# Optimization experiments

Measured on AMD Instinct MI355X. Metric: run time of the kernel, lower is better.

## Reference

```python
import jax, jax.numpy as jnp
from jax import lax
import numpy as np

EPS = 1e-8
B, SA, SB = 32, 64, 64
H, WD, L, V, CLS = 128, 300, 20, 50000, 3


def _div(n, d):
    # faithful to div_with_small_value: clamp denominator at EPS
    return n / jnp.where(d > EPS, d, EPS)


def _lstm(x, Wih, Whh, bih, bhh):
    # PyTorch gate order: i, f, g, o. x: [B, S, D] -> outputs [B, S, H], last h [B, H]
    def step(carry, xt):
        h, c = carry
        g = xt @ Wih.T + bih + h @ Whh.T + bhh
        i, f, gg, o = jnp.split(g, 4, axis=-1)
        c = jax.nn.sigmoid(f) * c + jax.nn.sigmoid(i) * jnp.tanh(gg)
        h = jax.nn.sigmoid(o) * jnp.tanh(c)
        return (h, c), h
    h0 = jnp.zeros((x.shape[0], Whh.shape[1]), x.dtype)
    (hT, _), hs = lax.scan(step, (h0, h0), jnp.swapaxes(x, 0, 1))
    return jnp.swapaxes(hs, 0, 1), hT


def _bilstm(x, pf, pb):
    of, _ = _lstm(x, *pf)
    ob, _ = _lstm(x[:, ::-1], *pb)
    return jnp.concatenate([of, ob[:, ::-1]], axis=-1)


def _full_match(v1, v2, w):
    # v1: [B,S,H]; v2: [B,H] or [B,S,H]; w: [L,H] -> [B,S,L]
    v1p = v1[:, :, None, :] * w
    v2p = (v2[:, None, None, :] if v2.ndim == 2 else v2[:, :, None, :]) * w
    num = jnp.sum(v1p * v2p, -1)
    den = jnp.linalg.norm(v1p, axis=-1) * jnp.linalg.norm(v2p, axis=-1)
    return _div(num, den)


def _maxpool_match(v1, v2, w):
    # cosine between every (i, j) pair under each perspective -> [B,SA,SB,L]
    v1p = v1[:, :, None, :] * w  # [B,SA,L,H]
    v2p = v2[:, :, None, :] * w  # [B,SB,L,H]
    num = jnp.einsum('bild,bjld->bijl', v1p, v2p)
    den = jnp.linalg.norm(v1p, axis=-1)[:, :, None, :] * jnp.linalg.norm(v2p, axis=-1)[:, None, :, :]
    return _div(num, den)


def _attention(v1, v2):
    # cosine similarity matrix [B,SA,SB]
    num = jnp.einsum('bid,bjd->bij', v1, v2)
    den = jnp.linalg.norm(v1, axis=-1)[:, :, None] * jnp.linalg.norm(v2, axis=-1)[:, None, :]
    return _div(num, den)


def setup_inputs():
    key = jax.random.key(0)
    ks = iter(jax.random.split(key, 64))
    def nrm(shape, s=0.05):
        return jax.random.normal(next(ks), shape, jnp.float32) * s
    inp = {
        'Atoken': jax.random.randint(next(ks), (B, SA), 0, V),
        'Btoken': jax.random.randint(next(ks), (B, SB), 0, V),
        'word_emb': nrm((V, WD), 0.1),
    }
    for d in ('f', 'b'):
        inp['ctx_Wih_' + d] = nrm((4 * H, WD))
        inp['ctx_Whh_' + d] = nrm((4 * H, H))
        inp['ctx_bih_' + d] = jnp.zeros(4 * H, jnp.float32)
        inp['ctx_bhh_' + d] = jnp.zeros(4 * H, jnp.float32)
        inp['agg_Wih_' + d] = nrm((4 * H, 8 * L))
        inp['agg_Whh_' + d] = nrm((4 * H, H))
        inp['agg_bih_' + d] = jnp.zeros(4 * H, jnp.float32)
        inp['agg_bhh_' + d] = jnp.zeros(4 * H, jnp.float32)
    for i in range(1, 9):
        inp['mp_w%d' % i] = nrm((L, H), 0.1)
    inp['fc1_W'] = nrm((2 * H, 4 * H))
    inp['fc1_b'] = jnp.zeros(2 * H, jnp.float32)
    inp['fc2_W'] = nrm((CLS, 2 * H))
    inp['fc2_b'] = jnp.zeros(CLS, jnp.float32)
    return inp


def reference(Atoken, Btoken, word_emb,
              ctx_Wih_f, ctx_Whh_f, ctx_bih_f, ctx_bhh_f,
              ctx_Wih_b, ctx_Whh_b, ctx_bih_b, ctx_bhh_b,
              mp_w1, mp_w2, mp_w3, mp_w4, mp_w5, mp_w6, mp_w7, mp_w8,
              agg_Wih_f, agg_Whh_f, agg_bih_f, agg_bhh_f,
              agg_Wih_b, agg_Whh_b, agg_bih_b, agg_bhh_b,
              fc1_W, fc1_b, fc2_W, fc2_b):
    A = word_emb[Atoken]   # [B,SA,WD]
    Bx = word_emb[Btoken]  # [B,SB,WD]
    pf = (ctx_Wih_f, ctx_Whh_f, ctx_bih_f, ctx_bhh_f)
    pb = (ctx_Wih_b, ctx_Whh_b, ctx_bih_b, ctx_bhh_b)
    cA = _bilstm(A, pf, pb)
    cB = _bilstm(Bx, pf, pb)
    cA_f, cA_b = cA[..., :H], cA[..., H:]
    cB_f, cB_b = cB[..., :H], cB[..., H:]

    # full matching against last fw / first bw states
    mvA_full_f = _full_match(cA_f, cB_f[:, -1], mp_w1)
    mvA_full_b = _full_match(cA_b, cB_b[:, 0], mp_w2)
    mvB_full_f = _full_match(cB_f, cA_f[:, -1], mp_w1)
    mvB_full_b = _full_match(cB_b, cA_b[:, 0], mp_w2)

    # max-pooling matching
    mm_f = _maxpool_match(cA_f, cB_f, mp_w3)  # [B,SA,SB,L]
    mm_b = _maxpool_match(cA_b, cB_b, mp_w4)
    mvA_max_f = mm_f.max(2); mvA_max_b = mm_b.max(2)
    mvB_max_f = mm_f.max(1); mvB_max_b = mm_b.max(1)

    # attentive matching
    att_f = _attention(cA_f, cB_f)  # [B,SA,SB]
    att_b = _attention(cA_b, cB_b)
    mean_B_f = _div(jnp.einsum('bij,bjd->bid', att_f, cB_f), att_f.sum(2, keepdims=True))
    mean_B_b = _div(jnp.einsum('bij,bjd->bid', att_b, cB_b), att_b.sum(2, keepdims=True))
    mean_A_f = _div(jnp.einsum('bij,bid->bjd', att_f, cA_f), att_f.sum(1)[:, :, None])
    mean_A_b = _div(jnp.einsum('bij,bid->bjd', att_b, cA_b), att_b.sum(1)[:, :, None])
    mvA_am_f = _full_match(cA_f, mean_B_f, mp_w5)
    mvA_am_b = _full_match(cA_b, mean_B_b, mp_w6)
    mvB_am_f = _full_match(cB_f, mean_A_f, mp_w5)
    mvB_am_b = _full_match(cB_b, mean_A_b, mp_w6)

    # attentive-max matching (broadcast-multiply-reduce, the headroom hotspot)
    max_B_f = jnp.max(cB_f[:, None, :, :] * att_f[..., None], axis=2)  # [B,SA,H]
    max_B_b = jnp.max(cB_b[:, None, :, :] * att_b[..., None], axis=2)
    max_A_f = jnp.max(cA_f[:, :, None, :] * att_f[..., None], axis=1)  # [B,SB,H]
    max_A_b = jnp.max(cA_b[:, :, None, :] * att_b[..., None], axis=1)
    mvA_ax_f = _full_match(cA_f, max_B_f, mp_w7)
    mvA_ax_b = _full_match(cA_b, max_B_b, mp_w8)
    mvB_ax_f = _full_match(cB_f, max_A_f, mp_w7)
    mvB_ax_b = _full_match(cB_b, max_A_b, mp_w8)

    mvA = jnp.concatenate([mvA_full_f, mvA_max_f, mvA_am_f, mvA_ax_f,
                           mvA_full_b, mvA_max_b, mvA_am_b, mvA_ax_b], axis=2)  # [B,SA,8L]
    mvB = jnp.concatenate([mvB_full_f, mvB_max_f, mvB_am_f, mvB_ax_f,
                           mvB_full_b, mvB_max_b, mvB_am_b, mvB_ax_b], axis=2)

    apf = (agg_Wih_f, agg_Whh_f, agg_bih_f, agg_bhh_f)
    apb = (agg_Wih_b, agg_Whh_b, agg_bih_b, agg_bhh_b)
    _, hAf = _lstm(mvA, *apf); _, hAb = _lstm(mvA[:, ::-1], *apb)
    _, hBf = _lstm(mvB, *apf); _, hBb = _lstm(mvB[:, ::-1], *apb)
    out = jnp.concatenate([hAf, hAb, hBf, hBb], axis=1)  # [B, 4H]
    out = jnp.tanh(out @ fc1_W.T + fc1_b)
    logits = out @ fc2_W.T + fc2_b
    return jax.nn.softmax(logits, axis=-1)
```

## Files before the change

### kernel.cpp

```cpp
#include <hip/hip_runtime.h>
#include <math.h>


#define EPSV 1e-8f

__device__ __forceinline__ float sigm(float x) { return 1.f / (1.f + __expf(-x)); }
__device__ __forceinline__ float tanh_f(float x) {
    float t = expm1f(-2.f * fabsf(x));
    float r = -t / (t + 2.f);
    return copysignf(r, x);
}
__device__ __forceinline__ float divg(float n, float d) { return n / (d > EPSV ? d : EPSV); }

template<bool GATHER>
__global__ __launch_bounds__(256)
void gemm_gin(const float* __restrict__ X,
              const int* __restrict__ tokA, const int* __restrict__ tokB,
              const float* __restrict__ emb,
              const float* __restrict__ Wf, const float* __restrict__ Wb,
              const float* __restrict__ bihF, const float* __restrict__ bhhF,
              const float* __restrict__ bihB, const float* __restrict__ bhhB,
              int K, float* __restrict__ Gout)
{
    const int tid = threadIdx.x;
    const int tx = tid & 15, ty = tid >> 4;
    const int m0 = blockIdx.x * 64;
    const int n0 = blockIdx.y * 64;
    const int dir = (n0 >= 512) ? 1 : 0;
    const float* Wd = dir ? Wb : Wf;
    const int nn0 = n0 & 511;

    __shared__ __align__(16) float As[100 * 68];
    __shared__ __align__(16) float Bs[100 * 68];

    float acc[4][4];
#pragma unroll
    for (int r = 0; r < 4; ++r)
#pragma unroll
        for (int c = 0; c < 4; ++c) acc[r][c] = 0.f;

    for (int k0 = 0; k0 < K; k0 += 100) {
        int kc = K - k0; if (kc > 100) kc = 100;
        for (int e = tid; e < 64 * kc; e += 256) {
            int r = e / kc, c = e - r * kc;
            int m = m0 + r;
            const float* xrow;
            if (GATHER) {
                int tok = (m < 2048) ? tokA[m] : tokB[m - 2048];
                xrow = emb + (size_t)tok * 300;
            } else {
                xrow = X + (size_t)m * K;
            }
            As[c * 68 + r] = xrow[k0 + c];
        }
        for (int e = tid; e < 64 * kc; e += 256) {
            int r = e / kc, c = e - r * kc;
            Bs[c * 68 + r] = Wd[(size_t)(nn0 + r) * K + k0 + c];
        }
        __syncthreads();
#pragma unroll 4
        for (int k = 0; k < kc; ++k) {
            float4 a = *(const float4*)(As + k * 68 + (ty << 2));
            float4 b = *(const float4*)(Bs + k * 68 + (tx << 2));
            acc[0][0] += a.x * b.x; acc[0][1] += a.x * b.y; acc[0][2] += a.x * b.z; acc[0][3] += a.x * b.w;
            acc[1][0] += a.y * b.x; acc[1][1] += a.y * b.y; acc[1][2] += a.y * b.z; acc[1][3] += a.y * b.w;
            acc[2][0] += a.z * b.x; acc[2][1] += a.z * b.y; acc[2][2] += a.z * b.z; acc[2][3] += a.z * b.w;
            acc[3][0] += a.w * b.x; acc[3][1] += a.w * b.y; acc[3][2] += a.w * b.z; acc[3][3] += a.w * b.w;
        }
        __syncthreads();
    }

    const float* bih = dir ? bihB : bihF;
    const float* bhh = dir ? bhhB : bhhF;
    const int chain = ((m0 >= 2048) ? 2 : 0) + dir;
    const int nn = nn0 + (tx << 2);
    float b0 = bih[nn] + bhh[nn];
    float b1 = bih[nn + 1] + bhh[nn + 1];
    float b2 = bih[nn + 2] + bhh[nn + 2];
    float b3 = bih[nn + 3] + bhh[nn + 3];
#pragma unroll
    for (int r = 0; r < 4; ++r) {
        int m = m0 + (ty << 2) + r;
        int row = m & 2047;
        float4 o;
        o.x = acc[r][0] + b0; o.y = acc[r][1] + b1; o.z = acc[r][2] + b2; o.w = acc[r][3] + b3;
        *(float4*)(Gout + ((size_t)chain * 2048 + row) * 512 + nn) = o;
    }
}

__global__ __launch_bounds__(512, 2)
void lstm_kernel(const float* __restrict__ Gin,
                 const float* __restrict__ WhhF, const float* __restrict__ WhhB,
                 float* __restrict__ outH, float* __restrict__ hfin, int storeAll)
{
    const int tid = threadIdx.x;
    const int chain = blockIdx.x >> 5;
    const int b = blockIdx.x & 31;
    const int rev = chain & 1;
    const float* Whh = rev ? WhhB : WhhF;

    __shared__ float4 hs4[32];
    __shared__ float gact[512];
    float* hs = (float*)hs4;

    float4 w4[32];
    const float4* wrow = (const float4*)(Whh + (size_t)tid * 128);
#pragma unroll
    for (int q = 0; q < 32; ++q) w4[q] = wrow[q];

    if (tid < 32) hs4[tid] = make_float4(0.f, 0.f, 0.f, 0.f);
    float c_reg = 0.f;
    __syncthreads();

    const size_t base = ((size_t)chain * 32 + b) * 64;
    float gin_cur = Gin[(base + (rev ? 63 : 0)) * 512 + tid];

    for (int t = 0; t < 64; ++t) {
        const int s_cur = rev ? 63 - t : t;
        float gin_next = 0.f;
        if (t + 1 < 64) {
            int s_next = rev ? 62 - t : t + 1;
            gin_next = Gin[(base + s_next) * 512 + tid];
        }
        float a0 = 0.f, a1 = 0.f, a2 = 0.f, a3 = 0.f;
#pragma unroll
        for (int q = 0; q < 32; ++q) {
            float4 h4 = hs4[q];
            a0 += h4.x * w4[q].x; a1 += h4.y * w4[q].y;
            a2 += h4.z * w4[q].z; a3 += h4.w * w4[q].w;
        }
        float g = gin_cur + ((a0 + a1) + (a2 + a3));
        gact[tid] = ((tid >> 7) == 2) ? tanh_f(g) : sigm(g);
        __syncthreads();
        if (tid < 128) {
            float iv = gact[tid], fv = gact[128 + tid], gv = gact[256 + tid], ov = gact[384 + tid];
            c_reg = fv * c_reg + iv * gv;
            float hv = ov * tanh_f(c_reg);
            hs[tid] = hv;
            if (storeAll) outH[(base + s_cur) * 128 + tid] = hv;
        }
        __syncthreads();
        gin_cur = gin_next;
    }
    if (!storeAll && tid < 128) hfin[(size_t)b * 512 + chain * 128 + tid] = hs[tid];
}

__global__ __launch_bounds__(256)
void attn_kernel(const float* __restrict__ ctxH, float* __restrict__ att)
{
    const int tid = threadIdx.x;
    const int b = blockIdx.x;
    const int dir = blockIdx.y;
    const float* cA = ctxH + (((size_t)dir * 32 + b) * 64) * 128;
    const float* cB = ctxH + (((size_t)(2 + dir) * 32 + b) * 64) * 128;
    __shared__ __align__(16) float sa[64 * 132];
    __shared__ __align__(16) float sb[64 * 132];
    __shared__ float na[64], nb[64];

    for (int e = tid; e < 8192; e += 256) {
        int i = e >> 7, k = e & 127;
        sa[i * 132 + k] = cA[e];
        sb[i * 132 + k] = cB[e];
    }
    __syncthreads();
    if (tid < 64) {
        float s = 0.f;
        for (int k = 0; k < 128; ++k) { float v = sa[tid * 132 + k]; s += v * v; }
        na[tid] = sqrtf(s);
    } else if (tid < 128) {
        int j = tid - 64; float s = 0.f;
        for (int k = 0; k < 128; ++k) { float v = sb[j * 132 + k]; s += v * v; }
        nb[j] = sqrtf(s);
    }
    __syncthreads();

    const int tx = tid & 15, ty = tid >> 4;
    float acc[4][4] = {};
    for (int k4 = 0; k4 < 32; ++k4) {
        float4 av[4], bv[4];
#pragma unroll
        for (int r = 0; r < 4; ++r) av[r] = *(const float4*)(sa + ((ty << 2) + r) * 132 + (k4 << 2));
#pragma unroll
        for (int c = 0; c < 4; ++c) bv[c] = *(const float4*)(sb + ((tx << 2) + c) * 132 + (k4 << 2));
#pragma unroll
        for (int r = 0; r < 4; ++r)
#pragma unroll
            for (int c = 0; c < 4; ++c)
                acc[r][c] += av[r].x * bv[c].x + av[r].y * bv[c].y + av[r].z * bv[c].z + av[r].w * bv[c].w;
    }
    float* attb = att + (((size_t)dir * 32 + b) * 64) * 64;
#pragma unroll
    for (int r = 0; r < 4; ++r) {
        int i = (ty << 2) + r;
#pragma unroll
        for (int c = 0; c < 4; ++c) {
            int j = (tx << 2) + c;
            attb[i * 64 + j] = divg(acc[r][c], na[i] * nb[j]);
        }
    }
}

__global__ __launch_bounds__(256)
void meanmax_kernel(const float* __restrict__ ctxH, const float* __restrict__ att,
                    float* __restrict__ meanB, float* __restrict__ meanA,
                    float* __restrict__ maxB, float* __restrict__ maxA)
{
    const int tid = threadIdx.x;
    const int b = blockIdx.x, dir = blockIdx.y, side = blockIdx.z;
    __shared__ float sat[64 * 68];
    __shared__ __align__(16) float sc[64 * 132];
    __shared__ float ssum[64];

    const float* attb = att + (((size_t)dir * 32 + b) * 64) * 64;
    const int chain_src = side ? dir : (2 + dir);
    const float* cS = ctxH + (((size_t)chain_src * 32 + b) * 64) * 128;

    for (int e = tid; e < 4096; e += 256) sat[(e >> 6) * 68 + (e & 63)] = attb[e];
    for (int e = tid; e < 8192; e += 256) sc[(e >> 7) * 132 + (e & 127)] = cS[e];
    __syncthreads();
    if (tid < 64) {
        float s = 0.f;
        for (int q = 0; q < 64; ++q) s += side ? sat[q * 68 + tid] : sat[tid * 68 + q];
        ssum[tid] = s;
    }
    __syncthreads();

    const int r = tid >> 2;
    const int d0 = (tid & 3) * 32;
    float4 am[8], axv[8];
#pragma unroll
    for (int p = 0; p < 8; ++p) {
        am[p] = make_float4(0.f, 0.f, 0.f, 0.f);
        axv[p] = make_float4(-INFINITY, -INFINITY, -INFINITY, -INFINITY);
    }
    for (int q = 0; q < 64; ++q) {
        float a = side ? sat[q * 68 + r] : sat[r * 68 + q];
#pragma unroll
        for (int p = 0; p < 8; ++p) {
            float4 cv = *(const float4*)(sc + q * 132 + d0 + (p << 2));
            float px = a * cv.x, py = a * cv.y, pz = a * cv.z, pw = a * cv.w;
            am[p].x += px; am[p].y += py; am[p].z += pz; am[p].w += pw;
            axv[p].x = fmaxf(axv[p].x, px); axv[p].y = fmaxf(axv[p].y, py);
            axv[p].z = fmaxf(axv[p].z, pz); axv[p].w = fmaxf(axv[p].w, pw);
        }
    }
    float den = ssum[r] > EPSV ? ssum[r] : EPSV;
    float inv = 1.f / den;
    float* mout = (side ? meanA : meanB) + (((size_t)dir * 32 + b) * 64 + r) * 128 + d0;
    float* xout = (side ? maxA : maxB) + (((size_t)dir * 32 + b) * 64 + r) * 128 + d0;
#pragma unroll
    for (int p = 0; p < 8; ++p) {
        float4 o;
        o.x = am[p].x * inv; o.y = am[p].y * inv; o.z = am[p].z * inv; o.w = am[p].w * inv;
        *(float4*)(mout + (p << 2)) = o;
        *(float4*)(xout + (p << 2)) = axv[p];
    }
}

__global__ __launch_bounds__(256)
void mm_kernel(const float* __restrict__ ctxH,
               const float* __restrict__ mpw3, const float* __restrict__ mpw4,
               float* __restrict__ mvA, float* __restrict__ mvB)
{
    const int tid = threadIdx.x;
    const int b = blockIdx.x, l = blockIdx.y, dir = blockIdx.z;
    const float* wsrc = (dir ? mpw4 : mpw3) + (size_t)l * 128;
    __shared__ float wl[128];
    __shared__ __align__(16) float su[64 * 132];
    __shared__ __align__(16) float sv[64 * 132];
    __shared__ float nu[64], nv[64];
    __shared__ float smm[64 * 68];

    const float* cA = ctxH + (((size_t)dir * 32 + b) * 64) * 128;
    const float* cB = ctxH + (((size_t)(2 + dir) * 32 + b) * 64) * 128;

    if (tid < 128) wl[tid] = wsrc[tid];
    __syncthreads();
    for (int e = tid; e < 8192; e += 256) {
        int i = e >> 7, k = e & 127;
        float w = wl[k];
        su[i * 132 + k] = cA[e] * w;
        sv[i * 132 + k] = cB[e] * w;
    }
    __syncthreads();
    if (tid < 64) {
        float s = 0.f;
        for (int k = 0; k < 128; ++k) { float v = su[tid * 132 + k]; s += v * v; }
        nu[tid] = sqrtf(s);
    } else if (tid < 128) {
        int j = tid - 64; float s = 0.f;
        for (int k = 0; k < 128; ++k) { float v = sv[j * 132 + k]; s += v * v; }
        nv[j] = sqrtf(s);
    }
    __syncthreads();

    const int tx = tid & 15, ty = tid >> 4;
    float acc[4][4] = {};
    for (int k4 = 0; k4 < 32; ++k4) {
        float4 av[4], bv[4];
#pragma unroll
        for (int r = 0; r < 4; ++r) av[r] = *(const float4*)(su + ((ty << 2) + r) * 132 + (k4 << 2));
#pragma unroll
        for (int c = 0; c < 4; ++c) bv[c] = *(const float4*)(sv + ((tx << 2) + c) * 132 + (k4 << 2));
#pragma unroll
        for (int r = 0; r < 4; ++r)
#pragma unroll
            for (int c = 0; c < 4; ++c)
                acc[r][c] += av[r].x * bv[c].x + av[r].y * bv[c].y + av[r].z * bv[c].z + av[r].w * bv[c].w;
    }
#pragma unroll
    for (int r = 0; r < 4; ++r) {
        int i = (ty << 2) + r;
#pragma unroll
        for (int c = 0; c < 4; ++c) {
            int j = (tx << 2) + c;
            smm[i * 68 + j] = divg(acc[r][c], nu[i] * nv[j]);
        }
    }
    __syncthreads();
    const int blkoff = (dir ? 5 : 1) * 20 + l;
    if (tid < 64) {
        float mx = -INFINITY;
        for (int j = 0; j < 64; ++j) mx = fmaxf(mx, smm[tid * 68 + j]);
        mvA[((size_t)b * 64 + tid) * 160 + blkoff] = mx;
    } else if (tid < 128) {
        int j = tid - 64;
        float mx = -INFINITY;
        for (int i = 0; i < 64; ++i) mx = fmaxf(mx, smm[i * 68 + j]);
        mvB[((size_t)b * 64 + j) * 160 + blkoff] = mx;
    }
}

__global__ __launch_bounds__(256)
void fm_kernel(const float* __restrict__ ctxH,
               const float* __restrict__ meanB, const float* __restrict__ meanA,
               const float* __restrict__ maxB, const float* __restrict__ maxA,
               const float* __restrict__ w1, const float* __restrict__ w2,
               const float* __restrict__ w5, const float* __restrict__ w6,
               const float* __restrict__ w7, const float* __restrict__ w8,
               float* __restrict__ mvA, float* __restrict__ mvB)
{
    const int tid = threadIdx.x;
    const int b = blockIdx.x, dir = blockIdx.y, side = blockIdx.z;
    __shared__ __align__(16) float sc[64 * 132];
    __shared__ __align__(16) float st[64 * 132];
    __shared__ __align__(16) float sw[20 * 132];

    const int chain_self = side ? (2 + dir) : dir;
    const float* cX = ctxH + (((size_t)chain_self * 32 + b) * 64) * 128;
    for (int e = tid; e < 8192; e += 256) sc[(e >> 7) * 132 + (e & 127)] = cX[e];

    for (int kind = 0; kind < 3; ++kind) {
        const float* w = (kind == 0) ? (dir ? w2 : w1)
                       : (kind == 1) ? (dir ? w6 : w5)
                                     : (dir ? w8 : w7);
        __syncthreads();
        if (kind == 0) {
            const int chain_o = side ? dir : (2 + dir);
            const float* trow = ctxH + (((size_t)chain_o * 32 + b) * 64 + (dir ? 0 : 63)) * 128;
            for (int e = tid; e < 128; e += 256) st[e] = trow[e];
        } else {
            const float* tsrc = (kind == 1) ? (side ? meanA : meanB) : (side ? maxA : maxB);
            tsrc += (((size_t)dir * 32 + b) * 64) * 128;
            for (int e = tid; e < 8192; e += 256) st[(e >> 7) * 132 + (e & 127)] = tsrc[e];
        }
        for (int e = tid; e < 2560; e += 256) sw[(e >> 7) * 132 + (e & 127)] = w[e];
        __syncthreads();

        const int blk = ((kind == 0) ? 0 : (kind == 1) ? 2 : 3) + (dir ? 4 : 0);
        float* mv = side ? mvB : mvA;
        for (int o = tid; o < 1280; o += 256) {
            int i = o / 20;
            int l = o - i * 20;
            const float* crow = sc + i * 132;
            const float* trow = st + ((kind == 0) ? 0 : i * 132);
            const float* wrow = sw + l * 132;
            float num = 0.f, na = 0.f, nb = 0.f;
#pragma unroll 8
            for (int k4 = 0; k4 < 32; ++k4) {
                float4 a = *(const float4*)(crow + (k4 << 2));
                float4 t = *(const float4*)(trow + (k4 << 2));
                float4 wv = *(const float4*)(wrow + (k4 << 2));
                float ax = a.x * wv.x, ay = a.y * wv.y, az = a.z * wv.z, aw = a.w * wv.w;
                float tx_ = t.x * wv.x, ty_ = t.y * wv.y, tz_ = t.z * wv.z, tw_ = t.w * wv.w;
                num += ax * tx_ + ay * ty_ + az * tz_ + aw * tw_;
                na  += ax * ax  + ay * ay  + az * az  + aw * aw;
                nb  += tx_ * tx_ + ty_ * ty_ + tz_ * tz_ + tw_ * tw_;
            }
            float den = sqrtf(na) * sqrtf(nb);
            mv[((size_t)b * 64 + i) * 160 + blk * 20 + l] = divg(num, den);
        }
    }
}

__global__ __launch_bounds__(256)
void head_kernel(const float* __restrict__ hfin,
                 const float* __restrict__ fc1W, const float* __restrict__ fc1b,
                 const float* __restrict__ fc2W, const float* __restrict__ fc2b,
                 float* __restrict__ out)
{
    const int b = blockIdx.x, tid = threadIdx.x;
    __shared__ __align__(16) float sx[512];
    __shared__ float sy[256], sl[3];
    for (int e = tid; e < 512; e += 256) sx[e] = hfin[(size_t)b * 512 + e];
    __syncthreads();
    {
        float acc = fc1b[tid];
        const float4* wr = (const float4*)(fc1W + (size_t)tid * 512);
#pragma unroll 8
        for (int k4 = 0; k4 < 128; ++k4) {
            float4 w = wr[k4];
            float4 x = *(const float4*)(sx + (k4 << 2));
            acc += w.x * x.x + w.y * x.y + w.z * x.z + w.w * x.w;
        }
        sy[tid] = tanh_f(acc);
    }
    __syncthreads();
    if (tid < 3) {
        float acc = fc2b[tid];
        for (int n = 0; n < 256; ++n) acc += sy[n] * fc2W[tid * 256 + n];
        sl[tid] = acc;
    }
    __syncthreads();
    if (tid < 3) {
        float m = fmaxf(sl[0], fmaxf(sl[1], sl[2]));
        float e0 = expf(sl[0] - m), e1 = expf(sl[1] - m), e2 = expf(sl[2] - m);
        float s = e0 + e1 + e2;
        float v = (tid == 0) ? e0 : ((tid == 1) ? e1 : e2);
        out[b * 3 + tid] = v / s;
    }
}

extern "C" void kernel_launch(void* const* d_in, const int* in_sizes, int n_in,
                              void* d_out, int out_size, void* d_ws, size_t ws_size,
                              hipStream_t stream)
{
    const bool dictOrder = (n_in > 7 && in_sizes[7] == 81920);
    int iCtxWih[2], iCtxWhh[2], iCtxBih[2], iCtxBhh[2];
    int iAggWih[2], iAggWhh[2], iAggBih[2], iAggBhh[2];
    int iW[8], iFc1W, iFc1b, iFc2W, iFc2b;
    if (dictOrder) {
        iCtxWih[0] = 3;  iCtxWhh[0] = 4;  iCtxBih[0] = 5;  iCtxBhh[0] = 6;
        iAggWih[0] = 7;  iAggWhh[0] = 8;  iAggBih[0] = 9;  iAggBhh[0] = 10;
        iCtxWih[1] = 11; iCtxWhh[1] = 12; iCtxBih[1] = 13; iCtxBhh[1] = 14;
        iAggWih[1] = 15; iAggWhh[1] = 16; iAggBih[1] = 17; iAggBhh[1] = 18;
        for (int k = 0; k < 8; ++k) iW[k] = 19 + k;
        iFc1W = 27; iFc1b = 28; iFc2W = 29; iFc2b = 30;
    } else {
        iCtxWih[0] = 3;  iCtxWhh[0] = 4;  iCtxBih[0] = 5;  iCtxBhh[0] = 6;
        iCtxWih[1] = 7;  iCtxWhh[1] = 8;  iCtxBih[1] = 9;  iCtxBhh[1] = 10;
        for (int k = 0; k < 8; ++k) iW[k] = 11 + k;
        iAggWih[0] = 19; iAggWhh[0] = 20; iAggBih[0] = 21; iAggBhh[0] = 22;
        iAggWih[1] = 23; iAggWhh[1] = 24; iAggBih[1] = 25; iAggBhh[1] = 26;
        iFc1W = 27; iFc1b = 28; iFc2W = 29; iFc2b = 30;
    }

    const int*   tokA = (const int*)d_in[0];
    const int*   tokB = (const int*)d_in[1];
    const float* emb  = (const float*)d_in[2];
    const float* ctxWihF = (const float*)d_in[iCtxWih[0]];
    const float* ctxWihB = (const float*)d_in[iCtxWih[1]];
    const float* ctxWhhF = (const float*)d_in[iCtxWhh[0]];
    const float* ctxWhhB = (const float*)d_in[iCtxWhh[1]];
    const float* ctxBihF = (const float*)d_in[iCtxBih[0]];
    const float* ctxBihB = (const float*)d_in[iCtxBih[1]];
    const float* ctxBhhF = (const float*)d_in[iCtxBhh[0]];
    const float* ctxBhhB = (const float*)d_in[iCtxBhh[1]];
    const float* aggWihF = (const float*)d_in[iAggWih[0]];
    const float* aggWihB = (const float*)d_in[iAggWih[1]];
    const float* aggWhhF = (const float*)d_in[iAggWhh[0]];
    const float* aggWhhB = (const float*)d_in[iAggWhh[1]];
    const float* aggBihF = (const float*)d_in[iAggBih[0]];
    const float* aggBihB = (const float*)d_in[iAggBih[1]];
    const float* aggBhhF = (const float*)d_in[iAggBhh[0]];
    const float* aggBhhB = (const float*)d_in[iAggBhh[1]];
    const float* mw[8];
    for (int k = 0; k < 8; ++k) mw[k] = (const float*)d_in[iW[k]];
    const float* fc1W = (const float*)d_in[iFc1W];
    const float* fc1b = (const float*)d_in[iFc1b];
    const float* fc2W = (const float*)d_in[iFc2W];
    const float* fc2b = (const float*)d_in[iFc2b];

    float* Wp    = (float*)d_ws;
    float* Gin   = Wp;
    float* ctxH  = Gin + 4194304;
    float* attw  = ctxH + 1048576;
    float* meanB = attw + 262144;
    float* meanA = meanB + 524288;
    float* maxB  = meanA + 524288;
    float* maxA  = maxB + 524288;
    float* mv    = maxA + 524288;
    float* hfin  = mv + 655360;
    float* mvA   = mv;
    float* mvB   = mv + (size_t)2048 * 160;

    dim3 gGemm(64, 16);

    gemm_gin<true><<<gGemm, 256, 0, stream>>>(
        nullptr, tokA, tokB, emb, ctxWihF, ctxWihB,
        ctxBihF, ctxBhhF, ctxBihB, ctxBhhB, 300, Gin);

    lstm_kernel<<<128, 512, 0, stream>>>(Gin, ctxWhhF, ctxWhhB, ctxH, hfin, 1);

    attn_kernel<<<dim3(32, 2), 256, 0, stream>>>(ctxH, attw);

    meanmax_kernel<<<dim3(32, 2, 2), 256, 0, stream>>>(ctxH, attw, meanB, meanA, maxB, maxA);

    mm_kernel<<<dim3(32, 20, 2), 256, 0, stream>>>(ctxH, mw[2], mw[3], mvA, mvB);

    fm_kernel<<<dim3(32, 2, 2), 256, 0, stream>>>(ctxH, meanB, meanA, maxB, maxA,
        mw[0], mw[1], mw[4], mw[5], mw[6], mw[7], mvA, mvB);

    gemm_gin<false><<<gGemm, 256, 0, stream>>>(
        mv, nullptr, nullptr, nullptr, aggWihF, aggWihB,
        aggBihF, aggBhhF, aggBihB, aggBhhB, 160, Gin);

    lstm_kernel<<<128, 512, 0, stream>>>(Gin, aggWhhF, aggWhhB, ctxH, hfin, 0);

    head_kernel<<<32, 256, 0, stream>>>(hfin, fc1W, fc1b, fc2W, fc2b, (float*)d_out);

    (void)out_size; (void)ws_size;
}
```

Measured before the change: 558.3 us.

## Prefetch GEMM tiles into registers with float4 loads and 16-wide K tiles

Rewrites the input-projection GEMM's tile loading. Each thread now owns one row of A and one row of W and loads a float4 of the next 16-wide K slice into registers while the current slice is being multiplied from shared memory. This replaces the scalar strided loads, the per-element integer division and the per-element token lookup with a hoisted row pointer. The cost is one extra register-staged buffer and more frequent barriers per K, since the tiles are smaller.

```diff
diff --git a/kernel.cpp b/kernel.cpp
--- a/kernel.cpp
+++ b/kernel.cpp
@@ -30,8 +30,22 @@
     const float* Wd = dir ? Wb : Wf;
     const int nn0 = n0 & 511;
 
-    __shared__ __align__(16) float As[100 * 68];
-    __shared__ __align__(16) float Bs[100 * 68];
+    __shared__ __align__(16) float As[16][64];
+    __shared__ __align__(16) float Bs[16][64];
+
+    const int sm = tid & 63;
+    const int sq = tid >> 6;
+    const int kq_off = sq << 2;
+
+    const float* arow;
+    if (GATHER) {
+        const int mg = m0 + sm;
+        const int tok = (mg < 2048) ? tokA[mg] : tokB[mg - 2048];
+        arow = emb + (size_t)tok * 300;
+    } else {
+        arow = X + (size_t)(m0 + sm) * K;
+    }
+    const float* brow = Wd + (size_t)(nn0 + sm) * K;
 
     float acc[4][4];
 #pragma unroll
@@ -39,35 +53,45 @@
 #pragma unroll
         for (int c = 0; c < 4; ++c) acc[r][c] = 0.f;
 
-    for (int k0 = 0; k0 < K; k0 += 100) {
-        int kc = K - k0; if (kc > 100) kc = 100;
-        for (int e = tid; e < 64 * kc; e += 256) {
-            int r = e / kc, c = e - r * kc;
-            int m = m0 + r;
-            const float* xrow;
-            if (GATHER) {
-                int tok = (m < 2048) ? tokA[m] : tokB[m - 2048];
-                xrow = emb + (size_t)tok * 300;
-            } else {
-                xrow = X + (size_t)m * K;
-            }
-            As[c * 68 + r] = xrow[k0 + c];
-        }
-        for (int e = tid; e < 64 * kc; e += 256) {
-            int r = e / kc, c = e - r * kc;
-            Bs[c * 68 + r] = Wd[(size_t)(nn0 + r) * K + k0 + c];
-        }
+    float4 av = make_float4(0.f, 0.f, 0.f, 0.f);
+    float4 bv = make_float4(0.f, 0.f, 0.f, 0.f);
+    {
+        const int kq = kq_off;
+        if (kq + 4 <= K) {
+            av = *(const float4*)(arow + kq);
+            bv = *(const float4*)(brow + kq);
+        }
+    }
+
+    for (int k0 = 0; k0 < K; k0 += 16) {
         __syncthreads();
-#pragma unroll 4
-        for (int k = 0; k < kc; ++k) {
-            float4 a = *(const float4*)(As + k * 68 + (ty << 2));
-            float4 b = *(const float4*)(Bs + k * 68 + (tx << 2));
+        As[kq_off + 0][sm] = av.x;
+        As[kq_off + 1][sm] = av.y;
+        As[kq_off + 2][sm] = av.z;
+        As[kq_off + 3][sm] = av.w;
+        Bs[kq_off + 0][sm] = bv.x;
+        Bs[kq_off + 1][sm] = bv.y;
+        Bs[kq_off + 2][sm] = bv.z;
+        Bs[kq_off + 3][sm] = bv.w;
+        __syncthreads();
+
+        av = make_float4(0.f, 0.f, 0.f, 0.f);
+        bv = make_float4(0.f, 0.f, 0.f, 0.f);
+        const int kq = k0 + 16 + kq_off;
+        if (kq + 4 <= K) {
+            av = *(const float4*)(arow + kq);
+            bv = *(const float4*)(brow + kq);
+        }
+
+#pragma unroll
+        for (int k = 0; k < 16; ++k) {
+            float4 a = *(const float4*)(&As[k][ty << 2]);
+            float4 b = *(const float4*)(&Bs[k][tx << 2]);
             acc[0][0] += a.x * b.x; acc[0][1] += a.x * b.y; acc[0][2] += a.x * b.z; acc[0][3] += a.x * b.w;
             acc[1][0] += a.y * b.x; acc[1][1] += a.y * b.y; acc[1][2] += a.y * b.z; acc[1][3] += a.y * b.w;
             acc[2][0] += a.z * b.x; acc[2][1] += a.z * b.y; acc[2][2] += a.z * b.z; acc[2][3] += a.z * b.w;
             acc[3][0] += a.w * b.x; acc[3][1] += a.w * b.y; acc[3][2] += a.w * b.z; acc[3][3] += a.w * b.w;
         }
-        __syncthreads();
     }
 
     const float* bih = dir ? bihB : bihF;
```

Result: faster. 490.1 us (-12.2%).
